# Kernel tuning notes

Hardware: AMD Instinct MI355X
Metric: run time of the kernel (lower is better)

## Reference

```python
import jax, jax.numpy as jnp
import numpy as np

N_NODES = 10000
N_EDGES = 320000
K = 5
C_IN = 128
C_OUT = 128


def setup_inputs() -> dict:
    key = jax.random.key(0)
    k_h, k_x, k_w, k_b = jax.random.split(key, 4)
    h = jax.random.normal(k_h, (N_NODES, C_IN), dtype=jnp.float32)
    X = jax.random.normal(k_x, (N_EDGES, K), dtype=jnp.float32)
    weight = jax.random.normal(k_w, (K, C_IN, C_OUT), dtype=jnp.float32) * 0.05
    bias = jax.random.normal(k_b, (C_OUT,), dtype=jnp.float32)
    # Unique (src, dst) pairs so scatter-set == segment-sum (matches torch indexing assignment).
    rng = np.random.default_rng(0)
    lin = np.unique(rng.integers(0, N_NODES * N_NODES, size=int(N_EDGES * 1.3)))
    assert len(lin) >= N_EDGES
    lin = lin[:N_EDGES]
    edge_index = jnp.asarray(np.stack([lin // N_NODES, lin % N_NODES]), dtype=jnp.int64)
    batch_node = jnp.zeros((N_NODES,), dtype=jnp.float32)
    return {"h": h, "X": X, "edge_index": edge_index, "batch_node": batch_node,
            "weight": weight, "bias": bias}


def reference(h, X, edge_index, batch_node, weight, bias):
    # Original torch code scatters X.T into a dense (K, N, N) adjacency and does
    # res = A @ h; that equals, per order k:
    #   res[k, i, :] = sum_{e: src_e = i} X[e, k] * h[dst_e, :]
    # which we compute sparsely with segment_sum (edges are unique).
    N = h.shape[0]
    src = edge_index[0]
    dst = edge_index[1]
    h_dst = h[dst]  # [E, C_in] gathered destination features

    def per_k(xk):  # xk: [E] edge values for one order k
        return jax.ops.segment_sum(xk[:, None] * h_dst, src, num_segments=N)  # [N, C_in]

    res_k = jax.vmap(per_k, in_axes=1)(X)  # [K, N, C_in]
    out = jnp.einsum('kni,kio->no', res_k, weight) + bias  # [N, C_out]
    return out
```

## Files before the change

### kernel.cpp

```cpp
#include <hip/hip_runtime.h>

#define N_NODES 10000
#define N_EDGES 320000
#define KDIM 640
#define C_OUT 128

typedef __attribute__((ext_vector_type(8))) short short8;
typedef __attribute__((ext_vector_type(4))) float floatx4;
typedef __attribute__((ext_vector_type(2))) unsigned int uintx2;

__device__ __forceinline__ unsigned short f2bf(float f) {
    unsigned int b = __float_as_uint(f);
    b = (b + 0x7FFFu + ((b >> 16) & 1u)) >> 16;
    return (unsigned short)b;
}
__device__ __forceinline__ unsigned int pack2(float x, float y) {
    return (unsigned int)f2bf(x) | ((unsigned int)f2bf(y) << 16);
}
__device__ __forceinline__ float2 unpack2(unsigned int u) {
    float2 r;
    r.x = __uint_as_float(u << 16);
    r.y = __uint_as_float(u & 0xFFFF0000u);
    return r;
}

__global__ __launch_bounds__(256) void prep(
        const float* __restrict__ h, uintx2* __restrict__ hb4,
        const float* __restrict__ W, unsigned short* __restrict__ Wt,
        const int* __restrict__ src, int* __restrict__ offsets) {
    const int bid = blockIdx.x;
    const int tid = threadIdx.x;

    if (bid < 1250) {
        const int t = bid * 256 + tid;
        floatx4 v = __builtin_nontemporal_load(&((const floatx4*)h)[t]);
        uintx2 o;
        o.x = pack2(v.x, v.y);
        o.y = pack2(v.z, v.w);
        hb4[t] = o;
    } else if (bid < 1330) {
        __shared__ float tile[32][33];
        const int b = bid - 1250;
        const int k0 = (b % 20) * 32, o0 = (b / 20) * 32;
        const int tx = tid & 31, ty = tid >> 5;
#pragma unroll
        for (int i = 0; i < 4; ++i)
            tile[ty + 8 * i][tx] =
                __builtin_nontemporal_load(&W[(size_t)(k0 + ty + 8 * i) * C_OUT + o0 + tx]);
        __syncthreads();
#pragma unroll
        for (int i = 0; i < 4; ++i)
            Wt[(size_t)(o0 + ty + 8 * i) * KDIM + k0 + tx] = f2bf(tile[tx][ty + 8 * i]);
    } else {
        const int n = (bid - 1330) * 256 + tid;
        if (n > N_NODES) return;
        int lo = 0, hi = N_EDGES;
        while (lo < hi) {
            int mid = (lo + hi) >> 1;
            if (src[mid] < n) lo = mid + 1; else hi = mid;
        }
        offsets[n] = lo;
    }
}

__global__ __launch_bounds__(512, 4) void fused_spectconv(
        const unsigned int* __restrict__ h2,
        const float* __restrict__ X,
        const int* __restrict__ dst,
        const int* __restrict__ offsets,
        const unsigned short* __restrict__ Wt,
        const float* __restrict__ bias,
        float* __restrict__ out) {
    __shared__ unsigned short Rs[16][648];
    __shared__ unsigned short Bs[128][68];

    const int tid  = threadIdx.x;
    const int wv   = __builtin_amdgcn_readfirstlane(tid >> 6);
    const int lane = tid & 63;
    const int m0   = blockIdx.x * 16;

    for (int nn = 0; nn < 2; ++nn) {
        const int node = m0 + wv * 2 + nn;
        const int e0 = offsets[node];
        const int e1 = offsets[node + 1];

        float a0x=0,a0y=0, a1x=0,a1y=0, a2x=0,a2y=0, a3x=0,a3y=0, a4x=0,a4y=0;

        int e = e0;
        for (; e + 7 < e1; e += 8) {
            int d[8];
            unsigned int u[8];
#pragma unroll
            for (int q = 0; q < 8; ++q) d[q] = dst[e + q];
#pragma unroll
            for (int q = 0; q < 8; ++q)
                u[q] = h2[(size_t)d[q] * 64 + lane];
#pragma unroll
            for (int q = 0; q < 8; ++q) {
                const float* Xp = X + (size_t)(e + q) * 5;
                const float x0 = Xp[0], x1 = Xp[1], x2 = Xp[2], x3 = Xp[3], x4 = Xp[4];
                const float2 hv = unpack2(u[q]);
                a0x = fmaf(x0, hv.x, a0x); a0y = fmaf(x0, hv.y, a0y);
                a1x = fmaf(x1, hv.x, a1x); a1y = fmaf(x1, hv.y, a1y);
                a2x = fmaf(x2, hv.x, a2x); a2y = fmaf(x2, hv.y, a2y);
                a3x = fmaf(x3, hv.x, a3x); a3y = fmaf(x3, hv.y, a3y);
                a4x = fmaf(x4, hv.x, a4x); a4y = fmaf(x4, hv.y, a4y);
            }
        }
        for (; e < e1; ++e) {
            const int d = dst[e];
            const unsigned int u = h2[(size_t)d * 64 + lane];
            const float* Xp = X + (size_t)e * 5;
            const float x0 = Xp[0], x1 = Xp[1], x2 = Xp[2], x3 = Xp[3], x4 = Xp[4];
            const float2 hv = unpack2(u);
            a0x = fmaf(x0, hv.x, a0x); a0y = fmaf(x0, hv.y, a0y);
            a1x = fmaf(x1, hv.x, a1x); a1y = fmaf(x1, hv.y, a1y);
            a2x = fmaf(x2, hv.x, a2x); a2y = fmaf(x2, hv.y, a2y);
            a3x = fmaf(x3, hv.x, a3x); a3y = fmaf(x3, hv.y, a3y);
            a4x = fmaf(x4, hv.x, a4x); a4y = fmaf(x4, hv.y, a4y);
        }

        const int nrel = wv * 2 + nn;
        *(unsigned int*)&Rs[nrel][0 * 128 + 2 * lane] = pack2(a0x, a0y);
        *(unsigned int*)&Rs[nrel][1 * 128 + 2 * lane] = pack2(a1x, a1y);
        *(unsigned int*)&Rs[nrel][2 * 128 + 2 * lane] = pack2(a2x, a2y);
        *(unsigned int*)&Rs[nrel][3 * 128 + 2 * lane] = pack2(a3x, a3y);
        *(unsigned int*)&Rs[nrel][4 * 128 + 2 * lane] = pack2(a4x, a4y);
    }

    __syncthreads();

    const int col  = lane & 15;
    const int quad = lane >> 4;
    const int c0   = wv * 16;

    floatx4 acc = {0.f, 0.f, 0.f, 0.f};

#pragma unroll
    for (int chunk = 0; chunk < 10; ++chunk) {
        if (chunk) __syncthreads();
#pragma unroll
        for (int r = 0; r < 2; ++r) {
            const int c = r * 512 + tid;
            const int row = c >> 3, c8 = c & 7;
            *(short8*)&Bs[row][c8 * 8] =
                *(const short8*)(Wt + (size_t)row * KDIM + chunk * 64 + c8 * 8);
        }
        __syncthreads();

#pragma unroll
        for (int hh = 0; hh < 2; ++hh) {
            const short8 af = *(const short8*)&Rs[col][chunk * 64 + hh * 32 + quad * 8];
            const short8 bf = *(const short8*)&Bs[c0 + col][hh * 32 + quad * 8];
            acc = __builtin_amdgcn_mfma_f32_16x16x32_bf16(af, bf, acc, 0, 0, 0);
        }
    }

    const float bv = bias[c0 + col];
#pragma unroll
    for (int r = 0; r < 4; ++r) {
        const int m = m0 + quad * 4 + r;
        __builtin_nontemporal_store(acc[r] + bv, &out[(size_t)m * C_OUT + c0 + col]);
    }
}

extern "C" void kernel_launch(void* const* d_in, const int* in_sizes, int n_in,
                              void* d_out, int out_size, void* d_ws, size_t ws_size,
                              hipStream_t stream) {
    const float* h      = (const float*)d_in[0];
    const float* X      = (const float*)d_in[1];
    const int*   ei     = (const int*)d_in[2];
    const float* weight = (const float*)d_in[4];
    const float* bias   = (const float*)d_in[5];
    float* out = (float*)d_out;

    const int* src = ei;
    const int* dst = ei + N_EDGES;

    char* wsb = (char*)d_ws;
    int*            offsets = (int*)wsb;
    uintx2*         hb4     = (uintx2*)(wsb + (64 << 10));
    unsigned short* Wtb     = (unsigned short*)(wsb + (64 << 10) + (4 << 20));

    prep<<<1370, 256, 0, stream>>>(h, hb4, weight, Wtb, src, offsets);
    fused_spectconv<<<625, 512, 0, stream>>>((const unsigned int*)hb4, X, dst,
                                             offsets, Wtb, bias, out);
}
```

Baseline: 100.2 us.

## Fuse prep kernel into main kernel, gathering fp32 h and converting W on the fly

Removes the separate prep launch. Each block now computes its own CSR offsets by binary search into shared memory. The gather reads h directly in fp32 instead of a prepacked bf16 copy, which doubles gather bytes but drops the conversion pass. The fp32 weight is transposed and converted to bf16 per chunk inside every block, which adds redundant global reads and conversion work across 625 blocks in exchange for one fewer launch and no workspace round-trip.

```diff
diff --git a/kernel.cpp b/kernel.cpp
--- a/kernel.cpp
+++ b/kernel.cpp
@@ -2,12 +2,12 @@
 
 #define N_NODES 10000
 #define N_EDGES 320000
+#define C_IN 128
+#define C_OUT 128
 #define KDIM 640
-#define C_OUT 128
 
 typedef __attribute__((ext_vector_type(8))) short short8;
 typedef __attribute__((ext_vector_type(4))) float floatx4;
-typedef __attribute__((ext_vector_type(2))) unsigned int uintx2;
 
 __device__ __forceinline__ unsigned short f2bf(float f) {
     unsigned int b = __float_as_uint(f);
@@ -17,115 +17,81 @@
 __device__ __forceinline__ unsigned int pack2(float x, float y) {
     return (unsigned int)f2bf(x) | ((unsigned int)f2bf(y) << 16);
 }
-__device__ __forceinline__ float2 unpack2(unsigned int u) {
-    float2 r;
-    r.x = __uint_as_float(u << 16);
-    r.y = __uint_as_float(u & 0xFFFF0000u);
-    return r;
-}
 
-__global__ __launch_bounds__(256) void prep(
-        const float* __restrict__ h, uintx2* __restrict__ hb4,
-        const float* __restrict__ W, unsigned short* __restrict__ Wt,
-        const int* __restrict__ src, int* __restrict__ offsets) {
-    const int bid = blockIdx.x;
+__global__ __launch_bounds__(512, 4) void fused_spectconv(
+        const float* __restrict__ h,
+        const float* __restrict__ X,
+        const int* __restrict__ dst,
+        const int* __restrict__ src,
+        const float* __restrict__ W,
+        const float* __restrict__ bias,
+        float* __restrict__ out) {
+    __shared__ int offs[17];
+    __shared__ unsigned short Rs[16][650];
+    __shared__ unsigned short Bs[128][66];
+
     const int tid = threadIdx.x;
+    const int m0  = blockIdx.x * 16;
 
-    if (bid < 1250) {
-        const int t = bid * 256 + tid;
-        floatx4 v = __builtin_nontemporal_load(&((const floatx4*)h)[t]);
-        uintx2 o;
-        o.x = pack2(v.x, v.y);
-        o.y = pack2(v.z, v.w);
-        hb4[t] = o;
-    } else if (bid < 1330) {
-        __shared__ float tile[32][33];
-        const int b = bid - 1250;
-        const int k0 = (b % 20) * 32, o0 = (b / 20) * 32;
-        const int tx = tid & 31, ty = tid >> 5;
-#pragma unroll
-        for (int i = 0; i < 4; ++i)
-            tile[ty + 8 * i][tx] =
-                __builtin_nontemporal_load(&W[(size_t)(k0 + ty + 8 * i) * C_OUT + o0 + tx]);
-        __syncthreads();
-#pragma unroll
-        for (int i = 0; i < 4; ++i)
-            Wt[(size_t)(o0 + ty + 8 * i) * KDIM + k0 + tx] = f2bf(tile[tx][ty + 8 * i]);
-    } else {
-        const int n = (bid - 1330) * 256 + tid;
-        if (n > N_NODES) return;
+    if (tid < 17) {
+        const int n = m0 + tid;
         int lo = 0, hi = N_EDGES;
         while (lo < hi) {
-            int mid = (lo + hi) >> 1;
+            const int mid = (lo + hi) >> 1;
             if (src[mid] < n) lo = mid + 1; else hi = mid;
         }
-        offsets[n] = lo;
+        offs[tid] = lo;
     }
-}
+    __syncthreads();
 
-__global__ __launch_bounds__(512, 4) void fused_spectconv(
-        const unsigned int* __restrict__ h2,
-        const float* __restrict__ X,
-        const int* __restrict__ dst,
-        const int* __restrict__ offsets,
-        const unsigned short* __restrict__ Wt,
-        const float* __restrict__ bias,
-        float* __restrict__ out) {
-    __shared__ unsigned short Rs[16][648];
-    __shared__ unsigned short Bs[128][68];
-
-    const int tid  = threadIdx.x;
     const int wv   = __builtin_amdgcn_readfirstlane(tid >> 6);
     const int lane = tid & 63;
-    const int m0   = blockIdx.x * 16;
+    const float2* __restrict__ hf2 = (const float2*)h;
 
     for (int nn = 0; nn < 2; ++nn) {
-        const int node = m0 + wv * 2 + nn;
-        const int e0 = offsets[node];
-        const int e1 = offsets[node + 1];
+        const int idx = wv * 2 + nn;
+        const int e0 = __builtin_amdgcn_readfirstlane(offs[idx]);
+        const int e1 = __builtin_amdgcn_readfirstlane(offs[idx + 1]);
 
         float a0x=0,a0y=0, a1x=0,a1y=0, a2x=0,a2y=0, a3x=0,a3y=0, a4x=0,a4y=0;
 
         int e = e0;
         for (; e + 7 < e1; e += 8) {
             int d[8];
-            unsigned int u[8];
+            float2 u[8];
 #pragma unroll
             for (int q = 0; q < 8; ++q) d[q] = dst[e + q];
 #pragma unroll
             for (int q = 0; q < 8; ++q)
-                u[q] = h2[(size_t)d[q] * 64 + lane];
+                u[q] = hf2[(size_t)d[q] * 64 + lane];
 #pragma unroll
             for (int q = 0; q < 8; ++q) {
                 const float* Xp = X + (size_t)(e + q) * 5;
                 const float x0 = Xp[0], x1 = Xp[1], x2 = Xp[2], x3 = Xp[3], x4 = Xp[4];
-                const float2 hv = unpack2(u[q]);
-                a0x = fmaf(x0, hv.x, a0x); a0y = fmaf(x0, hv.y, a0y);
-                a1x = fmaf(x1, hv.x, a1x); a1y = fmaf(x1, hv.y, a1y);
-                a2x = fmaf(x2, hv.x, a2x); a2y = fmaf(x2, hv.y, a2y);
-                a3x = fmaf(x3, hv.x, a3x); a3y = fmaf(x3, hv.y, a3y);
-                a4x = fmaf(x4, hv.x, a4x); a4y = fmaf(x4, hv.y, a4y);
+                a0x = fmaf(x0, u[q].x, a0x); a0y = fmaf(x0, u[q].y, a0y);
+                a1x = fmaf(x1, u[q].x, a1x); a1y = fmaf(x1, u[q].y, a1y);
+                a2x = fmaf(x2, u[q].x, a2x); a2y = fmaf(x2, u[q].y, a2y);
+                a3x = fmaf(x3, u[q].x, a3x); a3y = fmaf(x3, u[q].y, a3y);
+                a4x = fmaf(x4, u[q].x, a4x); a4y = fmaf(x4, u[q].y, a4y);
             }
         }
         for (; e < e1; ++e) {
             const int d = dst[e];
-            const unsigned int u = h2[(size_t)d * 64 + lane];
+            const float2 u = hf2[(size_t)d * 64 + lane];
             const float* Xp = X + (size_t)e * 5;
             const float x0 = Xp[0], x1 = Xp[1], x2 = Xp[2], x3 = Xp[3], x4 = Xp[4];
-            const float2 hv = unpack2(u);
-            a0x = fmaf(x0, hv.x, a0x); a0y = fmaf(x0, hv.y, a0y);
-            a1x = fmaf(x1, hv.x, a1x); a1y = fmaf(x1, hv.y, a1y);
-            a2x = fmaf(x2, hv.x, a2x); a2y = fmaf(x2, hv.y, a2y);
-            a3x = fmaf(x3, hv.x, a3x); a3y = fmaf(x3, hv.y, a3y);
-            a4x = fmaf(x4, hv.x, a4x); a4y = fmaf(x4, hv.y, a4y);
+            a0x = fmaf(x0, u.x, a0x); a0y = fmaf(x0, u.y, a0y);
+            a1x = fmaf(x1, u.x, a1x); a1y = fmaf(x1, u.y, a1y);
+            a2x = fmaf(x2, u.x, a2x); a2y = fmaf(x2, u.y, a2y);
+            a3x = fmaf(x3, u.x, a3x); a3y = fmaf(x3, u.y, a3y);
+            a4x = fmaf(x4, u.x, a4x); a4y = fmaf(x4, u.y, a4y);
         }
 
-        const int nrel = wv * 2 + nn;
-        *(unsigned int*)&Rs[nrel][0 * 128 + 2 * lane] = pack2(a0x, a0y);
-        *(unsigned int*)&Rs[nrel][1 * 128 + 2 * lane] = pack2(a1x, a1y);
-        *(unsigned int*)&Rs[nrel][2 * 128 + 2 * lane] = pack2(a2x, a2y);
-        *(unsigned int*)&Rs[nrel][3 * 128 + 2 * lane] = pack2(a3x, a3y);
-        *(unsigned int*)&Rs[nrel][4 * 128 + 2 * lane] = pack2(a4x, a4y);
+        *(unsigned int*)&Rs[idx][0 * 128 + 2 * lane] = pack2(a0x, a0y);
+        *(unsigned int*)&Rs[idx][1 * 128 + 2 * lane] = pack2(a1x, a1y);
+        *(unsigned int*)&Rs[idx][2 * 128 + 2 * lane] = pack2(a2x, a2y);
+        *(unsigned int*)&Rs[idx][3 * 128 + 2 * lane] = pack2(a3x, a3y);
+        *(unsigned int*)&Rs[idx][4 * 128 + 2 * lane] = pack2(a4x, a4y);
     }
 
     __syncthreads();
@@ -136,15 +102,16 @@
 
     floatx4 acc = {0.f, 0.f, 0.f, 0.f};
 
-#pragma unroll
     for (int chunk = 0; chunk < 10; ++chunk) {
         if (chunk) __syncthreads();
 #pragma unroll
-        for (int r = 0; r < 2; ++r) {
-            const int c = r * 512 + tid;
-            const int row = c >> 3, c8 = c & 7;
-            *(short8*)&Bs[row][c8 * 8] =
-                *(const short8*)(Wt + (size_t)row * KDIM + chunk * 64 + c8 * 8);
+        for (int r = 0; r < 8; ++r) {
+            const int i  = r * 512 + tid;
+            const int o  = i & 127;
+            const int kp = i >> 7;
+            const float w0 = W[(size_t)(chunk * 64 + 2 * kp + 0) * C_OUT + o];
+            const float w1 = W[(size_t)(chunk * 64 + 2 * kp + 1) * C_OUT + o];
+            *(unsigned int*)&Bs[o][2 * kp] = pack2(w0, w1);
         }
         __syncthreads();
 
@@ -177,12 +144,5 @@
     const int* src = ei;
     const int* dst = ei + N_EDGES;
 
-    char* wsb = (char*)d_ws;
-    int*            offsets = (int*)wsb;
-    uintx2*         hb4     = (uintx2*)(wsb + (64 << 10));
-    unsigned short* Wtb     = (unsigned short*)(wsb + (64 << 10) + (4 << 20));
-
-    prep<<<1370, 256, 0, stream>>>(h, hb4, weight, Wtb, src, offsets);
-    fused_spectconv<<<625, 512, 0, stream>>>((const unsigned int*)hb4, X, dst,
-                                             offsets, Wtb, bias, out);
+    fused_spectconv<<<625, 512, 0, stream>>>(h, X, dst, src, weight, bias, out);
 }
```

Result: slower. 104.4 us (+4.2%).

## Split fused gather-GEMM into separate scatter and 64-row tiled MFMA GEMM kernels

Applied to the files above, without the earlier changes.

The fused kernel is split into two. A scatter kernel computes each node's five-order aggregated features, one wavefront per node, and writes them to a bf16 workspace buffer. A separate GEMM kernel then multiplies 64-row tiles of that buffer by the transposed weight using MFMA, with each wave accumulating all 128 output columns. This cuts how often the 160KB weight matrix is re-read (each block previously reloaded it for only 16 nodes) and frees the scatter phase from LDS and barrier limits on occupancy. In exchange it adds a roughly 12.8MB intermediate write and read plus an extra kernel launch.

```diff
diff --git a/kernel.cpp b/kernel.cpp
--- a/kernel.cpp
+++ b/kernel.cpp
@@ -2,8 +2,9 @@
 
 #define N_NODES 10000
 #define N_EDGES 320000
+#define C_IN 128
+#define C_OUT 128
 #define KDIM 640
-#define C_OUT 128
 
 typedef __attribute__((ext_vector_type(8))) short short8;
 typedef __attribute__((ext_vector_type(4))) float floatx4;
@@ -63,85 +64,94 @@
     }
 }
 
-__global__ __launch_bounds__(512, 4) void fused_spectconv(
+__global__ __launch_bounds__(256) void scatter(
         const unsigned int* __restrict__ h2,
         const float* __restrict__ X,
         const int* __restrict__ dst,
         const int* __restrict__ offsets,
-        const unsigned short* __restrict__ Wt,
-        const float* __restrict__ bias,
-        float* __restrict__ out) {
-    __shared__ unsigned short Rs[16][648];
-    __shared__ unsigned short Bs[128][68];
-
-    const int tid  = threadIdx.x;
-    const int wv   = __builtin_amdgcn_readfirstlane(tid >> 6);
-    const int lane = tid & 63;
-    const int m0   = blockIdx.x * 16;
-
-    for (int nn = 0; nn < 2; ++nn) {
-        const int node = m0 + wv * 2 + nn;
-        const int e0 = offsets[node];
-        const int e1 = offsets[node + 1];
-
-        float a0x=0,a0y=0, a1x=0,a1y=0, a2x=0,a2y=0, a3x=0,a3y=0, a4x=0,a4y=0;
-
-        int e = e0;
-        for (; e + 7 < e1; e += 8) {
-            int d[8];
-            unsigned int u[8];
-#pragma unroll
-            for (int q = 0; q < 8; ++q) d[q] = dst[e + q];
-#pragma unroll
-            for (int q = 0; q < 8; ++q)
-                u[q] = h2[(size_t)d[q] * 64 + lane];
-#pragma unroll
-            for (int q = 0; q < 8; ++q) {
-                const float* Xp = X + (size_t)(e + q) * 5;
-                const float x0 = Xp[0], x1 = Xp[1], x2 = Xp[2], x3 = Xp[3], x4 = Xp[4];
-                const float2 hv = unpack2(u[q]);
-                a0x = fmaf(x0, hv.x, a0x); a0y = fmaf(x0, hv.y, a0y);
-                a1x = fmaf(x1, hv.x, a1x); a1y = fmaf(x1, hv.y, a1y);
-                a2x = fmaf(x2, hv.x, a2x); a2y = fmaf(x2, hv.y, a2y);
-                a3x = fmaf(x3, hv.x, a3x); a3y = fmaf(x3, hv.y, a3y);
-                a4x = fmaf(x4, hv.x, a4x); a4y = fmaf(x4, hv.y, a4y);
-            }
-        }
-        for (; e < e1; ++e) {
-            const int d = dst[e];
-            const unsigned int u = h2[(size_t)d * 64 + lane];
-            const float* Xp = X + (size_t)e * 5;
+        unsigned int* __restrict__ R2) {
+    const int wv   = __builtin_amdgcn_readfirstlane(threadIdx.x >> 6);
+    const int lane = threadIdx.x & 63;
+    const int node = blockIdx.x * 4 + wv;
+
+    const int e0 = offsets[node];
+    const int e1 = offsets[node + 1];
+
+    float a0x=0,a0y=0, a1x=0,a1y=0, a2x=0,a2y=0, a3x=0,a3y=0, a4x=0,a4y=0;
+
+    int e = e0;
+    for (; e + 7 < e1; e += 8) {
+        int d[8];
+        unsigned int u[8];
+#pragma unroll
+        for (int q = 0; q < 8; ++q) d[q] = dst[e + q];
+#pragma unroll
+        for (int q = 0; q < 8; ++q)
+            u[q] = h2[(size_t)d[q] * 64 + lane];
+#pragma unroll
+        for (int q = 0; q < 8; ++q) {
+            const float* Xp = X + (size_t)(e + q) * 5;
             const float x0 = Xp[0], x1 = Xp[1], x2 = Xp[2], x3 = Xp[3], x4 = Xp[4];
-            const float2 hv = unpack2(u);
+            const float2 hv = unpack2(u[q]);
             a0x = fmaf(x0, hv.x, a0x); a0y = fmaf(x0, hv.y, a0y);
             a1x = fmaf(x1, hv.x, a1x); a1y = fmaf(x1, hv.y, a1y);
             a2x = fmaf(x2, hv.x, a2x); a2y = fmaf(x2, hv.y, a2y);
             a3x = fmaf(x3, hv.x, a3x); a3y = fmaf(x3, hv.y, a3y);
             a4x = fmaf(x4, hv.x, a4x); a4y = fmaf(x4, hv.y, a4y);
         }
-
-        const int nrel = wv * 2 + nn;
-        *(unsigned int*)&Rs[nrel][0 * 128 + 2 * lane] = pack2(a0x, a0y);
-        *(unsigned int*)&Rs[nrel][1 * 128 + 2 * lane] = pack2(a1x, a1y);
-        *(unsigned int*)&Rs[nrel][2 * 128 + 2 * lane] = pack2(a2x, a2y);
-        *(unsigned int*)&Rs[nrel][3 * 128 + 2 * lane] = pack2(a3x, a3y);
-        *(unsigned int*)&Rs[nrel][4 * 128 + 2 * lane] = pack2(a4x, a4y);
-    }
-
-    __syncthreads();
-
+    }
+    for (; e < e1; ++e) {
+        const int d = dst[e];
+        const unsigned int u = h2[(size_t)d * 64 + lane];
+        const float* Xp = X + (size_t)e * 5;
+        const float x0 = Xp[0], x1 = Xp[1], x2 = Xp[2], x3 = Xp[3], x4 = Xp[4];
+        const float2 hv = unpack2(u);
+        a0x = fmaf(x0, hv.x, a0x); a0y = fmaf(x0, hv.y, a0y);
+        a1x = fmaf(x1, hv.x, a1x); a1y = fmaf(x1, hv.y, a1y);
+        a2x = fmaf(x2, hv.x, a2x); a2y = fmaf(x2, hv.y, a2y);
+        a3x = fmaf(x3, hv.x, a3x); a3y = fmaf(x3, hv.y, a3y);
+        a4x = fmaf(x4, hv.x, a4x); a4y = fmaf(x4, hv.y, a4y);
+    }
+
+    unsigned int* Rn = R2 + (size_t)node * 320;
+    Rn[0 * 64 + lane] = pack2(a0x, a0y);
+    Rn[1 * 64 + lane] = pack2(a1x, a1y);
+    Rn[2 * 64 + lane] = pack2(a2x, a2y);
+    Rn[3 * 64 + lane] = pack2(a3x, a3y);
+    Rn[4 * 64 + lane] = pack2(a4x, a4y);
+}
+
+__global__ __launch_bounds__(256) void gemm(
+        const unsigned short* __restrict__ R,
+        const unsigned short* __restrict__ Wt,
+        const float* __restrict__ bias,
+        float* __restrict__ out) {
+    __shared__ unsigned short As[64][66];
+    __shared__ unsigned short Bs[128][66];
+
+    const int tid  = threadIdx.x;
+    const int wv   = tid >> 6;
+    const int lane = tid & 63;
     const int col  = lane & 15;
     const int quad = lane >> 4;
-    const int c0   = wv * 16;
-
-    floatx4 acc = {0.f, 0.f, 0.f, 0.f};
-
-#pragma unroll
+    const int m0   = blockIdx.x * 64;
+
+    floatx4 acc[8];
+#pragma unroll
+    for (int t = 0; t < 8; ++t) acc[t] = (floatx4){0.f, 0.f, 0.f, 0.f};
+
     for (int chunk = 0; chunk < 10; ++chunk) {
         if (chunk) __syncthreads();
 #pragma unroll
         for (int r = 0; r < 2; ++r) {
-            const int c = r * 512 + tid;
+            const int c = r * 256 + tid;
+            const int row = c >> 3, c8 = c & 7;
+            *(short8*)&As[row][c8 * 8] =
+                *(const short8*)(R + (size_t)(m0 + row) * KDIM + chunk * 64 + c8 * 8);
+        }
+#pragma unroll
+        for (int r = 0; r < 4; ++r) {
+            const int c = r * 256 + tid;
             const int row = c >> 3, c8 = c & 7;
             *(short8*)&Bs[row][c8 * 8] =
                 *(const short8*)(Wt + (size_t)row * KDIM + chunk * 64 + c8 * 8);
@@ -150,17 +160,25 @@
 
 #pragma unroll
         for (int hh = 0; hh < 2; ++hh) {
-            const short8 af = *(const short8*)&Rs[col][chunk * 64 + hh * 32 + quad * 8];
-            const short8 bf = *(const short8*)&Bs[c0 + col][hh * 32 + quad * 8];
-            acc = __builtin_amdgcn_mfma_f32_16x16x32_bf16(af, bf, acc, 0, 0, 0);
-        }
-    }
-
-    const float bv = bias[c0 + col];
-#pragma unroll
-    for (int r = 0; r < 4; ++r) {
-        const int m = m0 + quad * 4 + r;
-        __builtin_nontemporal_store(acc[r] + bv, &out[(size_t)m * C_OUT + c0 + col]);
+            const short8 af = *(const short8*)&As[wv * 16 + col][hh * 32 + quad * 8];
+#pragma unroll
+            for (int t = 0; t < 8; ++t) {
+                const short8 bf = *(const short8*)&Bs[t * 16 + col][hh * 32 + quad * 8];
+                acc[t] = __builtin_amdgcn_mfma_f32_16x16x32_bf16(af, bf, acc[t], 0, 0, 0);
+            }
+        }
+    }
+
+#pragma unroll
+    for (int t = 0; t < 8; ++t) {
+        const float bv = bias[t * 16 + col];
+#pragma unroll
+        for (int r = 0; r < 4; ++r) {
+            const int m = m0 + wv * 16 + quad * 4 + r;
+            if (m < N_NODES)
+                __builtin_nontemporal_store(acc[t][r] + bv,
+                                            &out[(size_t)m * C_OUT + t * 16 + col]);
+        }
     }
 }
 
@@ -181,8 +199,9 @@
     int*            offsets = (int*)wsb;
     uintx2*         hb4     = (uintx2*)(wsb + (64 << 10));
     unsigned short* Wtb     = (unsigned short*)(wsb + (64 << 10) + (4 << 20));
+    unsigned int*   R2      = (unsigned int*)(wsb + (64 << 10) + (8 << 20));
 
     prep<<<1370, 256, 0, stream>>>(h, hb4, weight, Wtb, src, offsets);
-    fused_spectconv<<<625, 512, 0, stream>>>((const unsigned int*)hb4, X, dst,
-                                             offsets, Wtb, bias, out);
-}
+    scatter<<<2500, 256, 0, stream>>>((const unsigned int*)hb4, X, dst, offsets, R2);
+    gemm<<<157, 256, 0, stream>>>((const unsigned short*)R2, Wtb, bias, out);
+}
```

Result: slower. 111.9 us (+11.7%).
